# Kernel tuning notes

Hardware: AMD Instinct MI355X
Metric: run time of the kernel (lower is better)

## Reference

```python
import jax, jax.numpy as jnp
from jax import lax
import numpy as np

B, T, F = 64, 128, 16
H = 512
S = 2  # num_seg; SEG_DICT['2'] = [8, 6], seg_cumsum = [2, 10, 16]


def timestep_embedding(t, dim, max_period=10000.0):
    half = dim // 2
    freqs = jnp.exp(-jnp.log(max_period) * jnp.arange(half, dtype=jnp.float32) / half)
    args = t[:, None] * freqs  # [N, half]
    return jnp.concatenate([jnp.cos(args), jnp.sin(args)], axis=-1)  # [N, dim]


def setup_inputs() -> dict:
    key = jax.random.key(0)
    ks = jax.random.split(key, 16)
    sc = lambda *sh: 1.0 / np.sqrt(sh[-1])
    inp = {
        'x': jax.random.normal(ks[0], (B, T, F), dtype=jnp.float32),
        'lengths': jax.random.randint(ks[1], (B,), 1, T + 1),
        'h0': jax.random.uniform(ks[2], (B, H), dtype=jnp.float32),
        'c0': jax.random.uniform(ks[3], (B, H), dtype=jnp.float32),
        'W_is0': jax.random.normal(ks[4], (H, 8), dtype=jnp.float32) * sc(8),
        'b_is0': jax.random.normal(ks[5], (H,), dtype=jnp.float32) * 0.01,
        'W_is1': jax.random.normal(ks[6], (H, 6), dtype=jnp.float32) * sc(6),
        'b_is1': jax.random.normal(ks[7], (H,), dtype=jnp.float32) * 0.01,
        'W_ih': jax.random.normal(ks[8], (4 * H, 3 * H), dtype=jnp.float32) * sc(3 * H),
        'W_hh': jax.random.normal(ks[9], (4 * H, H), dtype=jnp.float32) * sc(H),
        'b_ih': jax.random.normal(ks[10], (4 * H,), dtype=jnp.float32) * 0.01,
        'b_hh': jax.random.normal(ks[11], (4 * H,), dtype=jnp.float32) * 0.01,
        'W_o': jax.random.normal(ks[12], (F - 2, S * H), dtype=jnp.float32) * sc(S * H),
        'b_o': jax.random.normal(ks[13], (F - 2,), dtype=jnp.float32) * 0.01,
    }
    return inp


def reference(x, lengths, h0, c0, W_is0, b_is0, W_is1, b_is1,
              W_ih, W_hh, b_ih, b_hh, W_o, b_o):
    b, t, f = x.shape
    h = h0.shape[1]
    xf = x.reshape(-1, f)  # [B*T, F]

    # timestep embeddings from the two time columns (learning_type='diff')
    tc = timestep_embedding(xf[:, 0], h)
    tp = timestep_embedding(xf[:, 1], h)
    t_emb = jnp.concatenate([tc, tp], axis=-1)  # [B*T, 2H]

    # per-segment input linears (segments = cols 2:10 and 10:16)
    e0 = xf[:, 2:10] @ W_is0.T + b_is0
    e1 = xf[:, 10:16] @ W_is1.T + b_is1
    e0 = jnp.concatenate([e0, t_emb], axis=-1)[:, None, :]  # [B*T, 1, 3H]
    e1 = jnp.concatenate([e1, t_emb], axis=-1)[:, None, :]
    # faithful to torch: concat on dim=1 then reshape(batch, num_seg, seq_len, -1)
    embs = jnp.concatenate([e0, e1], axis=1).reshape(b, S, t, 3 * h)

    def cell(carry, xt):
        hh, cc = carry
        gates = xt @ W_ih.T + b_ih + hh @ W_hh.T + b_hh
        i, fg, g, o = jnp.split(gates, 4, axis=-1)  # torch LSTMCell order i,f,g,o
        cc = jax.nn.sigmoid(fg) * cc + jax.nn.sigmoid(i) * jnp.tanh(g)
        hh = jax.nn.sigmoid(o) * jnp.tanh(cc)
        return (hh, cc), hh

    hs = []
    for s in range(S):  # shared cell weights across segments (same nn.LSTMCell object)
        xs = jnp.swapaxes(embs[:, s], 0, 1)  # [T, B, 3H]
        _, h_seq = lax.scan(cell, (h0, c0), xs)  # [T, B, H]
        hs.append(jnp.swapaxes(h_seq, 0, 1))  # [B, T, H]
    hidden_states = jnp.stack(hs, axis=-2)  # [B, T, S, H]; dropout rate 0 -> identity

    idx = lengths - 1  # final valid timestep per sequence
    hfin = hidden_states[jnp.arange(b), idx].reshape(b, S * h)  # [B, S*H]
    out = jax.nn.sigmoid(hfin @ W_o.T + b_o)  # mlp_o: Linear + Sigmoid
    return out
```

## Files before the change

kernel.cpp:

```cpp
#include <hip/hip_runtime.h>
#include <hip/hip_bf16.h>
#include <stdint.h>


typedef __attribute__((ext_vector_type(8))) short bf16x8_t;
typedef __attribute__((ext_vector_type(4))) float f32x4_t;

#define SENT 0xAAAAAAAAu

#define OFF_G      0u
#define OFF_TEMB   33554432u
#define OFF_HH     50331648u
#define OFF_WHH    67239936u
#define OFF_WMID   69337088u
#define OFF_WC0    73531392u
#define OFF_WC1    73596928u
#define OFF_BC     73662464u
#define OFF_HFIN   73678848u

__device__ __forceinline__ float bf2f(uint16_t u){
  union { uint32_t i; float f; } v; v.i = ((uint32_t)u) << 16; return v.f;
}
__device__ __forceinline__ uint16_t f2b(float f){
  union { float f; uint32_t i; } v; v.f = f;
  uint32_t r = v.i + 0x7fffu + ((v.i >> 16) & 1u);
  return (uint16_t)(r >> 16);
}
__device__ __forceinline__ float sigm(float x){ return 1.0f/(1.0f + __expf(-x)); }
__device__ __forceinline__ float tanh_(float x){
  float xc = fminf(fmaxf(x, -15.f), 15.f);
  float t = __expf(2.f*xc);
  return (t - 1.f)/(t + 1.f);
}
__device__ __forceinline__ void gl_lds16(const void* g, void* l){
  __builtin_amdgcn_global_load_lds(
      (const __attribute__((address_space(1))) void*)g,
      (__attribute__((address_space(3))) void*)l, 16, 0, 0);
}

__global__ void prep1(const float* __restrict__ W_ih, const float* __restrict__ W_hh,
                      const float* __restrict__ W_is0, const float* __restrict__ b_is0,
                      const float* __restrict__ W_is1, const float* __restrict__ b_is1,
                      const float* __restrict__ b_ih, const float* __restrict__ b_hh,
                      uint16_t* __restrict__ whh_b, uint16_t* __restrict__ wmid_b,
                      float* __restrict__ wc0, float* __restrict__ wc1, float* __restrict__ bc){
  const int n = blockIdx.x;
  const int tid = threadIdx.x;
  __shared__ float wrow[512];
  __shared__ float red[16][17];
  wrow[tid]       = W_ih[(size_t)n*1536 + tid];
  wrow[tid + 256] = W_ih[(size_t)n*1536 + 256 + tid];
  for (int j = tid; j < 1024; j += 256)
    wmid_b[(size_t)n*1024 + j] = f2b(W_ih[(size_t)n*1536 + 512 + j]);
  for (int k = tid; k < 512; k += 256)
    whh_b[(size_t)n*512 + k] = f2b(W_hh[(size_t)n*512 + k]);
  __syncthreads();
  {
    const int d = tid >> 4, jp = tid & 15;
    float s = 0.f;
    const int kk0 = jp*32;
    if (d < 8){
      for (int k = kk0; k < kk0 + 32; ++k) s += wrow[k]*W_is0[k*8 + d];
    } else if (d < 14){
      int c = d - 8;
      for (int k = kk0; k < kk0 + 32; ++k) s += wrow[k]*W_is1[k*6 + c];
    } else if (d == 14){
      for (int k = kk0; k < kk0 + 32; ++k) s += wrow[k]*b_is0[k];
    } else {
      for (int k = kk0; k < kk0 + 32; ++k) s += wrow[k]*b_is1[k];
    }
    red[d][jp] = s;
  }
  __syncthreads();
  if (tid < 16){
    float tot = 0.f;
    #pragma unroll
    for (int i = 0; i < 16; ++i) tot += red[tid][i];
    if (tid < 8)       wc0[n*8 + tid] = tot;
    else if (tid < 14) wc1[n*8 + (tid - 8)] = tot;
    else if (tid == 14) bc[n]        = b_ih[n] + b_hh[n] + tot;
    else                bc[2048 + n] = b_ih[n] + b_hh[n] + tot;
  } else if (tid == 16){
    wc1[n*8 + 6] = 0.f; wc1[n*8 + 7] = 0.f;
  }
}

__global__ void prep2(const float* __restrict__ h0, uint16_t* __restrict__ h_hist){
  int i = blockIdx.x*256 + threadIdx.x;
  uint32_t* hh = (uint32_t*)h_hist;
  if (i < 32768){
    int e    = i*2;
    int rrcg = e >> 9;
    int rr   = rrcg >> 4, cg = rrcg & 15;
    int rm   = e & 511;
    int row  = rm >> 5, u = rm & 31;
    int b    = (rr*16 + row) & 63;
    int unit = cg*32 + u;
    uint32_t lo = f2b(h0[(size_t)b*512 + unit]);
    uint32_t hi = f2b(h0[(size_t)b*512 + unit + 1]);
    uint32_t wd = lo | (hi << 16);
    if (wd == SENT) wd ^= 1u;
    hh[i] = wd;
  } else if (i < 4227072){
    hh[i] = SENT;
  }
}

__global__ void tembk(const float* __restrict__ x, uint16_t* __restrict__ temb){
  const int rid = blockIdx.x;
  const int k = threadIdx.x;
  float x0 = x[(size_t)rid*16 + 0], x1 = x[(size_t)rid*16 + 1];
  float f = __expf((float)k * (-9.210340371976184f/256.f));
  float a0 = x0*f, a1 = x1*f;
  size_t base = (size_t)rid*1024;
  temb[base + k]        = f2b(__cosf(a0));
  temb[base + 256 + k]  = f2b(__sinf(a0));
  temb[base + 512 + k]  = f2b(__cosf(a1));
  temb[base + 768 + k]  = f2b(__sinf(a1));
}

__launch_bounds__(256)
__global__ void gemmB(const uint16_t* __restrict__ temb, const uint16_t* __restrict__ wmid,
                      uint16_t* __restrict__ G){
  __shared__ __align__(16) uint16_t smem[16384];
  uint16_t* Al = smem;
  uint16_t* Bl = smem + 8192;
  const int tid = threadIdx.x;
  const int m0 = blockIdx.x*128, n0 = blockIdx.y*128;
  const int w = tid >> 6, lane = tid & 63;
  const int q = lane >> 4, ln = lane & 15;
  const int wm = w >> 1, wn = w & 1;
  const int srow_l = (lane >> 3);
  const int scol   = (lane & 7)*8;

  f32x4_t acc[4][4];
  #pragma unroll
  for (int a = 0; a < 4; ++a)
    #pragma unroll
    for (int b = 0; b < 4; ++b) acc[a][b] = (f32x4_t){0.f,0.f,0.f,0.f};

  for (int kb = 0; kb < 16; ++kb){
    #pragma unroll
    for (int i = 0; i < 4; ++i){
      int row0 = w*32 + i*8;
      int row  = row0 + srow_l;
      gl_lds16(temb + (size_t)(m0 + row)*1024 + kb*64 + scol, &Al[row0*64]);
      gl_lds16(wmid + (size_t)(n0 + row)*1024 + kb*64 + scol, &Bl[row0*64]);
    }
    __syncthreads();
    #pragma unroll
    for (int kc = 0; kc < 2; ++kc){
      bf16x8_t af[4], bf[4];
      #pragma unroll
      for (int mt = 0; mt < 4; ++mt)
        af[mt] = *(const bf16x8_t*)&Al[(wm*64 + mt*16 + ln)*64 + kc*32 + q*8];
      #pragma unroll
      for (int nt = 0; nt < 4; ++nt)
        bf[nt] = *(const bf16x8_t*)&Bl[(wn*64 + nt*16 + ln)*64 + kc*32 + q*8];
      #pragma unroll
      for (int mt = 0; mt < 4; ++mt)
        #pragma unroll
        for (int nt = 0; nt < 4; ++nt)
          acc[mt][nt] = __builtin_amdgcn_mfma_f32_16x16x32_bf16(af[mt], bf[nt], acc[mt][nt], 0, 0, 0);
    }
    __syncthreads();
  }

  #pragma unroll
  for (int mt = 0; mt < 4; ++mt)
    #pragma unroll
    for (int nt = 0; nt < 4; ++nt)
      #pragma unroll
      for (int r = 0; r < 4; ++r){
        int Mr = wm*64 + mt*16 + q*4 + r;
        int Nc = wn*64 + nt*16 + ln;
        smem[Mr*128 + Nc] = f2b(acc[mt][nt][r]);
      }
  __syncthreads();
  {
    const int erow = tid >> 1, eh = tid & 1;
    uint4* gdst = (uint4*)(G + (size_t)(m0 + erow)*2048 + n0 + eh*64);
    const uint4* lsrc = (const uint4*)&smem[erow*128 + eh*64];
    #pragma unroll
    for (int i2 = 0; i2 < 8; ++i2) gdst[i2] = lsrc[i2];
  }
}

__launch_bounds__(256)
__global__ void lstmk(const float* __restrict__ x, const float* __restrict__ c0,
                      const int* __restrict__ lengths,
                      const uint16_t* __restrict__ whh_b, const uint16_t* __restrict__ G,
                      const float* __restrict__ wc0, const float* __restrict__ wc1,
                      const float* __restrict__ bc,
                      uint16_t* __restrict__ h_hist, float* __restrict__ hfin){
  __shared__ __align__(16) uint16_t h_l[2][16][552];

  const int tid = threadIdx.x;
  const int bid = blockIdx.x;
  const int rr = bid & 7;
  const int g  = bid >> 3;
  const int k0 = g*32;
  const int sp = rr >> 2;
  const int w = tid >> 6, lane = tid & 63;
  const int q = lane >> 4, ln = lane & 15;
  const int u8 = ln & 7, gh = ln >> 3;
  const int unit = k0 + w*8 + u8;
  const int gl0 = gh*512 + unit;
  const int gl1 = (2 + gh)*512 + unit;

  const int LVL = 65536;

  bf16x8_t barr0[16], barr1[16];
  #pragma unroll
  for (int kc = 0; kc < 16; ++kc){
    barr0[kc] = *(const bf16x8_t*)(whh_b + (size_t)gl0*512 + kc*32 + q*8);
    barr1[kc] = *(const bf16x8_t*)(whh_b + (size_t)gl1*512 + kc*32 + q*8);
  }
  bf16x8_t e0f[2], e1f[2];
  #pragma unroll
  for (int nsI = 0; nsI < 2; ++nsI){
    bf16x8_t v0 = {0,0,0,0,0,0,0,0}, v1 = {0,0,0,0,0,0,0,0};
    if (q == 0){
      const float* wcs = nsI ? wc1 : wc0;
      #pragma unroll
      for (int jj = 0; jj < 8; ++jj){
        ((uint16_t*)&v0)[jj] = f2b(wcs[gl0*8 + jj]);
        ((uint16_t*)&v1)[jj] = f2b(wcs[gl1*8 + jj]);
      }
    }
    e0f[nsI] = v0; e1f[nsI] = v1;
  }
  float bc0v[2] = { bc[gl0], bc[2048 + gl0] };
  float bc1v[2] = { bc[gl1], bc[2048 + gl1] };

  int   bmr[4], lenr[4];
  float cst[4];
  #pragma unroll
  for (int r = 0; r < 4; ++r){
    int row = rr*16 + q*4 + r;
    bmr[r]  = row & 63;
    lenr[r] = lengths[bmr[r]];
    cst[r]  = c0[(size_t)bmr[r]*512 + unit];
  }

  const int prow = lane >> 2;
  const int pcol = (lane & 3)*8;
  const int xm = tid >> 3, xc = tid & 7;
  const int xb = (rr*16 + xm) & 63;

  const size_t stb = ((size_t)rr*8192 + g*512);

  for (int idx = tid; idx < 2*16*32; idx += 256)
    h_l[idx >> 9][(idx >> 5) & 15][520 + (idx & 31)] = 0;

  for (int t = 0; t < 128; ++t){
    const int qidx = sp*128 + t;
    const int ntm = qidx >> 1;
    const int ns  = qidx & 1;
    const int buf = t & 1;

    uint16_t g0r[4], g1r[4];
    #pragma unroll
    for (int r = 0; r < 4; ++r){
      size_t grow = (size_t)(bmr[r]*128 + ntm)*2048;
      g0r[r] = G[grow + gl0];
      g1r[r] = G[grow + gl1];
    }
    float xv = 0.f;
    if (tid < 128){
      if (ns == 0)      xv = x[(size_t)(xb*128 + ntm)*16 + 2 + xc];
      else if (xc < 6)  xv = x[(size_t)(xb*128 + ntm)*16 + 10 + xc];
    }

    {
      const unsigned long long* lvl = (const unsigned long long*)h_hist
                                      + (((size_t)t*LVL + (size_t)rr*8192) >> 2);
      unsigned long long hv[4][2];
      while (true){
        bool ok = true;
        #pragma unroll
        for (int i = 0; i < 4; ++i){
          const unsigned long long* p = lvl + ((size_t)(w*4 + i)*128 + prow*8 + (pcol >> 2));
          hv[i][0] = __hip_atomic_load(&p[0], __ATOMIC_RELAXED, __HIP_MEMORY_SCOPE_AGENT);
          hv[i][1] = __hip_atomic_load(&p[1], __ATOMIC_RELAXED, __HIP_MEMORY_SCOPE_AGENT);
          ok &= ((uint32_t)hv[i][0] != SENT) & ((uint32_t)(hv[i][0] >> 32) != SENT)
              & ((uint32_t)hv[i][1] != SENT) & ((uint32_t)(hv[i][1] >> 32) != SENT);
        }
        if (__all(ok)) break;
        __builtin_amdgcn_s_sleep(1);
      }
      #pragma unroll
      for (int i = 0; i < 4; ++i){
        int reg = w*4 + i;
        *(unsigned long long*)&h_l[buf][prow][reg*32 + pcol]     = hv[i][0];
        *(unsigned long long*)&h_l[buf][prow][reg*32 + pcol + 4] = hv[i][1];
      }
    }
    if (tid < 128) h_l[buf][xm][512 + xc] = f2b(xv);
    __syncthreads();

    f32x4_t acc0, acc1;
    {
      float b0 = ns ? bc0v[1] : bc0v[0];
      float b1 = ns ? bc1v[1] : bc1v[0];
      #pragma unroll
      for (int r = 0; r < 4; ++r){ acc0[r] = bf2f(g0r[r]) + b0; acc1[r] = bf2f(g1r[r]) + b1; }
    }
    #pragma unroll
    for (int kc = 0; kc < 16; ++kc){
      bf16x8_t a = *(const bf16x8_t*)&h_l[buf][ln][kc*32 + q*8];
      acc0 = __builtin_amdgcn_mfma_f32_16x16x32_bf16(a, barr0[kc], acc0, 0, 0, 0);
      acc1 = __builtin_amdgcn_mfma_f32_16x16x32_bf16(a, barr1[kc], acc1, 0, 0, 0);
    }
    {
      bf16x8_t a = *(const bf16x8_t*)&h_l[buf][ln][512 + q*8];
      acc0 = __builtin_amdgcn_mfma_f32_16x16x32_bf16(a, ns ? e0f[1] : e0f[0], acc0, 0, 0, 0);
      acc1 = __builtin_amdgcn_mfma_f32_16x16x32_bf16(a, ns ? e1f[1] : e1f[0], acc1, 0, 0, 0);
    }

    float pf[4], po[4];
    #pragma unroll
    for (int r = 0; r < 4; ++r){
      pf[r] = __shfl_xor(acc0[r], 8);
      po[r] = __shfl_xor(acc1[r], 8);
    }
    if (ln < 8){
      uint32_t hb[4]; float hF[4];
      #pragma unroll
      for (int r = 0; r < 4; ++r){
        float ig = acc0[r], fg = pf[r], gg = acc1[r], og = po[r];
        cst[r] = sigm(fg)*cst[r] + sigm(ig)*tanh_(gg);
        float h = sigm(og)*tanh_(cst[r]);
        hF[r] = h; hb[r] = (uint32_t)f2b(h);
      }
      #pragma unroll
      for (int r = 0; r < 4; ++r){
        uint32_t ph = (uint32_t)__shfl_xor((int)hb[r], 1);
        uint32_t packed = hb[r] | (ph << 16);
        if (packed == SENT) packed ^= 1u;
        uint32_t hi = (uint32_t)__shfl_xor((int)packed, 2);
        if ((ln & 3) == 0){
          unsigned long long v = (unsigned long long)packed | ((unsigned long long)hi << 32);
          unsigned long long* hp = (unsigned long long*)h_hist
              + (((size_t)(t+1)*LVL + stb + (size_t)(q*4 + r)*32 + w*8 + u8) >> 2);
          __hip_atomic_store(hp, v, __ATOMIC_RELAXED, __HIP_MEMORY_SCOPE_AGENT);
        }
        if (t == lenr[r] - 1)
          hfin[(size_t)bmr[r]*1024 + sp*512 + unit] = hF[r];
      }
    }
  }
}

__global__ void outk(const float* __restrict__ hfin, const float* __restrict__ W_o,
                     const float* __restrict__ b_o, float* __restrict__ out){
  __shared__ float hl[1024];
  __shared__ float red[16][17];
  const int b = blockIdx.x, tid = threadIdx.x;
  #pragma unroll
  for (int i = 0; i < 4; ++i) hl[tid + i*256] = hfin[(size_t)b*1024 + tid + i*256];
  __syncthreads();
  const int o = tid >> 4, j0 = tid & 15;
  float s = 0.f;
  if (o < 14){
    for (int j = j0; j < 1024; j += 16) s += hl[j]*W_o[(size_t)o*1024 + j];
  }
  red[o][j0] = s;
  __syncthreads();
  if (tid < 14){
    float tot = b_o[tid];
    #pragma unroll
    for (int i = 0; i < 16; ++i) tot += red[tid][i];
    out[b*14 + tid] = 1.0f/(1.0f + __expf(-tot));
  }
}

extern "C" void kernel_launch(void* const* d_in, const int* in_sizes, int n_in,
                              void* d_out, int out_size, void* d_ws, size_t ws_size,
                              hipStream_t stream){
  const float* x     = (const float*)d_in[0];
  const int*   lens  = (const int*)  d_in[1];
  const float* h0    = (const float*)d_in[2];
  const float* c0    = (const float*)d_in[3];
  const float* W_is0 = (const float*)d_in[4];
  const float* b_is0 = (const float*)d_in[5];
  const float* W_is1 = (const float*)d_in[6];
  const float* b_is1 = (const float*)d_in[7];
  const float* W_ih  = (const float*)d_in[8];
  const float* W_hh  = (const float*)d_in[9];
  const float* b_ih  = (const float*)d_in[10];
  const float* b_hh  = (const float*)d_in[11];
  const float* W_o   = (const float*)d_in[12];
  const float* b_o   = (const float*)d_in[13];
  float* out = (float*)d_out;

  char* ws = (char*)d_ws;
  uint16_t* G      = (uint16_t*)(ws + OFF_G);
  uint16_t* temb   = (uint16_t*)(ws + OFF_TEMB);
  uint16_t* h_hist = (uint16_t*)(ws + OFF_HH);
  uint16_t* whh_b  = (uint16_t*)(ws + OFF_WHH);
  uint16_t* wmid_b = (uint16_t*)(ws + OFF_WMID);
  float* wc0  = (float*)(ws + OFF_WC0);
  float* wc1  = (float*)(ws + OFF_WC1);
  float* bc   = (float*)(ws + OFF_BC);
  float* hfin = (float*)(ws + OFF_HFIN);

  hipLaunchKernelGGL(prep1, dim3(2048), dim3(256), 0, stream,
                     W_ih, W_hh, W_is0, b_is0, W_is1, b_is1, b_ih, b_hh,
                     whh_b, wmid_b, wc0, wc1, bc);
  hipLaunchKernelGGL(prep2, dim3(16512), dim3(256), 0, stream, h0, h_hist);
  hipLaunchKernelGGL(tembk, dim3(8192), dim3(256), 0, stream, x, temb);
  hipLaunchKernelGGL(gemmB, dim3(64, 16), dim3(256), 0, stream, temb, wmid_b, G);
  hipLaunchKernelGGL(lstmk, dim3(128), dim3(256), 0, stream,
                     x, c0, lens, whh_b, G, wc0, wc1, bc, h_hist, hfin);
  hipLaunchKernelGGL(outk, dim3(64), dim3(256), 0, stream, hfin, W_o, b_o, out);
}
```

Measured before the change: 590.4 us.

## Fuse GEMM into LSTM kernel with per-tile flags to overlap input projection

Merges the three prep kernels into one launch and folds the input-projection GEMM into the recurrent LSTM kernel. The first 128 blocks run the recurrence while the remaining blocks compute G tiles, each publishing a release flag that the recurrent blocks poll before consuming that tile. Tiles are reordered so timesteps needed first are produced early, and the G layout changes so rows are indexed by time then batch. This hides the GEMM behind the serial LSTM and removes launch gaps. The cost is spin-wait polling and a dependence on the GEMM blocks being scheduled alongside the persistent blocks.

After: 569.1 us. 1.04x faster.

```diff
diff --git a/kernel.cpp b/kernel.cpp
--- a/kernel.cpp
+++ b/kernel.cpp
@@ -17,6 +17,7 @@
 #define OFF_WC1    73596928u
 #define OFF_BC     73662464u
 #define OFF_HFIN   73678848u
+#define OFF_GFLAG  73940992u
 
 __device__ __forceinline__ float bf2f(uint16_t u){
   union { uint32_t i; float f; } v; v.i = ((uint32_t)u) << 16; return v.f;
@@ -38,57 +39,71 @@
       (__attribute__((address_space(3))) void*)l, 16, 0, 0);
 }
 
-__global__ void prep1(const float* __restrict__ W_ih, const float* __restrict__ W_hh,
-                      const float* __restrict__ W_is0, const float* __restrict__ b_is0,
-                      const float* __restrict__ W_is1, const float* __restrict__ b_is1,
-                      const float* __restrict__ b_ih, const float* __restrict__ b_hh,
-                      uint16_t* __restrict__ whh_b, uint16_t* __restrict__ wmid_b,
-                      float* __restrict__ wc0, float* __restrict__ wc1, float* __restrict__ bc){
-  const int n = blockIdx.x;
-  const int tid = threadIdx.x;
-  __shared__ float wrow[512];
-  __shared__ float red[16][17];
-  wrow[tid]       = W_ih[(size_t)n*1536 + tid];
-  wrow[tid + 256] = W_ih[(size_t)n*1536 + 256 + tid];
-  for (int j = tid; j < 1024; j += 256)
-    wmid_b[(size_t)n*1024 + j] = f2b(W_ih[(size_t)n*1536 + 512 + j]);
-  for (int k = tid; k < 512; k += 256)
-    whh_b[(size_t)n*512 + k] = f2b(W_hh[(size_t)n*512 + k]);
-  __syncthreads();
-  {
-    const int d = tid >> 4, jp = tid & 15;
-    float s = 0.f;
-    const int kk0 = jp*32;
-    if (d < 8){
-      for (int k = kk0; k < kk0 + 32; ++k) s += wrow[k]*W_is0[k*8 + d];
-    } else if (d < 14){
-      int c = d - 8;
-      for (int k = kk0; k < kk0 + 32; ++k) s += wrow[k]*W_is1[k*6 + c];
-    } else if (d == 14){
-      for (int k = kk0; k < kk0 + 32; ++k) s += wrow[k]*b_is0[k];
-    } else {
-      for (int k = kk0; k < kk0 + 32; ++k) s += wrow[k]*b_is1[k];
-    }
-    red[d][jp] = s;
-  }
-  __syncthreads();
-  if (tid < 16){
-    float tot = 0.f;
-    #pragma unroll
-    for (int i = 0; i < 16; ++i) tot += red[tid][i];
-    if (tid < 8)       wc0[n*8 + tid] = tot;
-    else if (tid < 14) wc1[n*8 + (tid - 8)] = tot;
-    else if (tid == 14) bc[n]        = b_ih[n] + b_hh[n] + tot;
-    else                bc[2048 + n] = b_ih[n] + b_hh[n] + tot;
-  } else if (tid == 16){
-    wc1[n*8 + 6] = 0.f; wc1[n*8 + 7] = 0.f;
-  }
-}
-
-__global__ void prep2(const float* __restrict__ h0, uint16_t* __restrict__ h_hist){
-  int i = blockIdx.x*256 + threadIdx.x;
-  uint32_t* hh = (uint32_t*)h_hist;
-  if (i < 32768){
+__global__ void prepAll(const float* __restrict__ x,
+                        const float* __restrict__ W_ih, const float* __restrict__ W_hh,
+                        const float* __restrict__ W_is0, const float* __restrict__ b_is0,
+                        const float* __restrict__ W_is1, const float* __restrict__ b_is1,
+                        const float* __restrict__ b_ih, const float* __restrict__ b_hh,
+                        const float* __restrict__ h0,
+                        uint16_t* __restrict__ whh_b, uint16_t* __restrict__ wmid_b,
+                        float* __restrict__ wc0, float* __restrict__ wc1,
+                        float* __restrict__ bc,
+                        uint16_t* __restrict__ temb, uint16_t* __restrict__ h_hist,
+                        uint32_t* __restrict__ gflag){
+  const int bid = blockIdx.x, tid = threadIdx.x;
+  if (bid < 2048){
+    const int n = bid;
+    __shared__ float wrow[512];
+    __shared__ float red[16][17];
+    wrow[tid]       = W_ih[(size_t)n*1536 + tid];
+    wrow[tid + 256] = W_ih[(size_t)n*1536 + 256 + tid];
+    for (int j = tid; j < 1024; j += 256)
+      wmid_b[(size_t)n*1024 + j] = f2b(W_ih[(size_t)n*1536 + 512 + j]);
+    for (int k = tid; k < 512; k += 256)
+      whh_b[(size_t)n*512 + k] = f2b(W_hh[(size_t)n*512 + k]);
+    __syncthreads();
+    {
+      const int d = tid >> 4, jp = tid & 15;
+      float s = 0.f;
+      const int kk0 = jp*32;
+      if (d < 8){
+        for (int k = kk0; k < kk0 + 32; ++k) s += wrow[k]*W_is0[k*8 + d];
+      } else if (d < 14){
+        int c = d - 8;
+        for (int k = kk0; k < kk0 + 32; ++k) s += wrow[k]*W_is1[k*6 + c];
+      } else if (d == 14){
+        for (int k = kk0; k < kk0 + 32; ++k) s += wrow[k]*b_is0[k];
+      } else {
+        for (int k = kk0; k < kk0 + 32; ++k) s += wrow[k]*b_is1[k];
+      }
+      red[d][jp] = s;
+    }
+    __syncthreads();
+    if (tid < 16){
+      float tot = 0.f;
+      #pragma unroll
+      for (int i = 0; i < 16; ++i) tot += red[tid][i];
+      if (tid < 8)        wc0[n*8 + tid] = tot;
+      else if (tid < 14)  wc1[n*8 + (tid - 8)] = tot;
+      else if (tid == 14) bc[n]        = b_ih[n] + b_hh[n] + tot;
+      else                bc[2048 + n] = b_ih[n] + b_hh[n] + tot;
+    } else if (tid == 16){
+      wc1[n*8 + 6] = 0.f; wc1[n*8 + 7] = 0.f;
+    }
+  } else if (bid < 10240){
+    const int rid = bid - 2048;
+    const int k = tid;
+    float x0 = x[(size_t)rid*16 + 0], x1 = x[(size_t)rid*16 + 1];
+    float f = __expf((float)k * (-9.210340371976184f/256.f));
+    float a0 = x0*f, a1 = x1*f;
+    size_t base = (size_t)rid*1024;
+    temb[base + k]        = f2b(__cosf(a0));
+    temb[base + 256 + k]  = f2b(__sinf(a0));
+    temb[base + 512 + k]  = f2b(__cosf(a1));
+    temb[base + 768 + k]  = f2b(__sinf(a1));
+  } else if (bid < 10368){
+    int i = (bid - 10240)*256 + tid;
+    uint32_t* hh = (uint32_t*)h_hist;
     int e    = i*2;
     int rrcg = e >> 9;
     int rr   = rrcg >> 4, cg = rrcg & 15;
@@ -101,113 +116,110 @@
     uint32_t wd = lo | (hi << 16);
     if (wd == SENT) wd ^= 1u;
     hh[i] = wd;
-  } else if (i < 4227072){
-    hh[i] = SENT;
-  }
-}
-
-__global__ void tembk(const float* __restrict__ x, uint16_t* __restrict__ temb){
-  const int rid = blockIdx.x;
-  const int k = threadIdx.x;
-  float x0 = x[(size_t)rid*16 + 0], x1 = x[(size_t)rid*16 + 1];
-  float f = __expf((float)k * (-9.210340371976184f/256.f));
-  float a0 = x0*f, a1 = x1*f;
-  size_t base = (size_t)rid*1024;
-  temb[base + k]        = f2b(__cosf(a0));
-  temb[base + 256 + k]  = f2b(__sinf(a0));
-  temb[base + 512 + k]  = f2b(__cosf(a1));
-  temb[base + 768 + k]  = f2b(__sinf(a1));
+    if (i < 1024) gflag[i] = 0u;
+  } else {
+    uint32_t* hh = (uint32_t*)h_hist;
+    size_t w0 = 32768u + ((size_t)(bid - 10368)*256 + tid)*8;
+    uint4 s4 = make_uint4(SENT, SENT, SENT, SENT);
+    *(uint4*)&hh[w0]     = s4;
+    *(uint4*)&hh[w0 + 4] = s4;
+  }
 }
 
 __launch_bounds__(256)
-__global__ void gemmB(const uint16_t* __restrict__ temb, const uint16_t* __restrict__ wmid,
-                      uint16_t* __restrict__ G){
-  __shared__ __align__(16) uint16_t smem[16384];
-  uint16_t* Al = smem;
-  uint16_t* Bl = smem + 8192;
+__global__ void fusedk(const float* __restrict__ x, const float* __restrict__ c0,
+                       const int* __restrict__ lengths,
+                       const uint16_t* __restrict__ whh_b, const uint16_t* __restrict__ temb,
+                       const uint16_t* __restrict__ wmid,
+                       const float* __restrict__ wc0, const float* __restrict__ wc1,
+                       const float* __restrict__ bc,
+                       uint16_t* __restrict__ G, uint16_t* __restrict__ h_hist,
+                       uint32_t* __restrict__ gflag, float* __restrict__ hfin){
+  __shared__ __align__(16) uint16_t smem_u[17664];
   const int tid = threadIdx.x;
-  const int m0 = blockIdx.x*128, n0 = blockIdx.y*128;
+  const int bid = blockIdx.x;
   const int w = tid >> 6, lane = tid & 63;
   const int q = lane >> 4, ln = lane & 15;
-  const int wm = w >> 1, wn = w & 1;
-  const int srow_l = (lane >> 3);
-  const int scol   = (lane & 7)*8;
-
-  f32x4_t acc[4][4];
-  #pragma unroll
-  for (int a = 0; a < 4; ++a)
-    #pragma unroll
-    for (int b = 0; b < 4; ++b) acc[a][b] = (f32x4_t){0.f,0.f,0.f,0.f};
-
-  for (int kb = 0; kb < 16; ++kb){
-    #pragma unroll
-    for (int i = 0; i < 4; ++i){
-      int row0 = w*32 + i*8;
-      int row  = row0 + srow_l;
-      gl_lds16(temb + (size_t)(m0 + row)*1024 + kb*64 + scol, &Al[row0*64]);
-      gl_lds16(wmid + (size_t)(n0 + row)*1024 + kb*64 + scol, &Bl[row0*64]);
-    }
+
+  if (bid >= 128){
+    const int gb = bid - 128;
+    const int idx = gb >> 4;
+    const int mt = (idx & 1) ? (idx >> 1) : (32 + (idx >> 1));
+    const int n0 = (gb & 15)*128;
+    uint16_t* Al = smem_u;
+    uint16_t* Bl = smem_u + 8192;
+    const int wm = w >> 1, wn = w & 1;
+    const int srow_l = lane >> 3, scol = (lane & 7)*8;
+
+    f32x4_t acc[4][4];
+    #pragma unroll
+    for (int a = 0; a < 4; ++a)
+      #pragma unroll
+      for (int b2 = 0; b2 < 4; ++b2) acc[a][b2] = (f32x4_t){0.f,0.f,0.f,0.f};
+
+    for (int kb = 0; kb < 16; ++kb){
+      #pragma unroll
+      for (int i = 0; i < 4; ++i){
+        int row0 = w*32 + i*8;
+        int lrow = row0 + srow_l;
+        int bA = lrow & 63, ntmA = mt*2 + (lrow >> 6);
+        gl_lds16(temb + (size_t)(bA*128 + ntmA)*1024 + kb*64 + scol, &Al[row0*64]);
+        gl_lds16(wmid + (size_t)(n0 + lrow)*1024 + kb*64 + scol, &Bl[row0*64]);
+      }
+      __syncthreads();
+      #pragma unroll
+      for (int kc = 0; kc < 2; ++kc){
+        bf16x8_t af[4], bf[4];
+        #pragma unroll
+        for (int mt_i = 0; mt_i < 4; ++mt_i)
+          af[mt_i] = *(const bf16x8_t*)&Al[(wm*64 + mt_i*16 + ln)*64 + kc*32 + q*8];
+        #pragma unroll
+        for (int nt = 0; nt < 4; ++nt)
+          bf[nt] = *(const bf16x8_t*)&Bl[(wn*64 + nt*16 + ln)*64 + kc*32 + q*8];
+        #pragma unroll
+        for (int mt_i = 0; mt_i < 4; ++mt_i)
+          #pragma unroll
+          for (int nt = 0; nt < 4; ++nt)
+            acc[mt_i][nt] = __builtin_amdgcn_mfma_f32_16x16x32_bf16(af[mt_i], bf[nt], acc[mt_i][nt], 0, 0, 0);
+      }
+      __syncthreads();
+    }
+    #pragma unroll
+    for (int mt_i = 0; mt_i < 4; ++mt_i)
+      #pragma unroll
+      for (int nt = 0; nt < 4; ++nt)
+        #pragma unroll
+        for (int r = 0; r < 4; ++r){
+          int Mr = wm*64 + mt_i*16 + q*4 + r;
+          int Nc = wn*64 + nt*16 + ln;
+          smem_u[Mr*128 + Nc] = f2b(acc[mt_i][nt][r]);
+        }
     __syncthreads();
-    #pragma unroll
-    for (int kc = 0; kc < 2; ++kc){
-      bf16x8_t af[4], bf[4];
-      #pragma unroll
-      for (int mt = 0; mt < 4; ++mt)
-        af[mt] = *(const bf16x8_t*)&Al[(wm*64 + mt*16 + ln)*64 + kc*32 + q*8];
-      #pragma unroll
-      for (int nt = 0; nt < 4; ++nt)
-        bf[nt] = *(const bf16x8_t*)&Bl[(wn*64 + nt*16 + ln)*64 + kc*32 + q*8];
-      #pragma unroll
-      for (int mt = 0; mt < 4; ++mt)
-        #pragma unroll
-        for (int nt = 0; nt < 4; ++nt)
-          acc[mt][nt] = __builtin_amdgcn_mfma_f32_16x16x32_bf16(af[mt], bf[nt], acc[mt][nt], 0, 0, 0);
+    {
+      const int erow = tid >> 1, eh = tid & 1;
+      const unsigned long long* lsrc = (const unsigned long long*)&smem_u[erow*128 + eh*64];
+      unsigned long long* gdst = (unsigned long long*)
+          (G + (size_t)(mt*128 + erow)*2048 + n0 + eh*64);
+      #pragma unroll
+      for (int i2 = 0; i2 < 16; ++i2)
+        __hip_atomic_store(&gdst[i2], lsrc[i2], __ATOMIC_RELAXED, __HIP_MEMORY_SCOPE_AGENT);
     }
     __syncthreads();
-  }
-
-  #pragma unroll
-  for (int mt = 0; mt < 4; ++mt)
-    #pragma unroll
-    for (int nt = 0; nt < 4; ++nt)
-      #pragma unroll
-      for (int r = 0; r < 4; ++r){
-        int Mr = wm*64 + mt*16 + q*4 + r;
-        int Nc = wn*64 + nt*16 + ln;
-        smem[Mr*128 + Nc] = f2b(acc[mt][nt][r]);
-      }
-  __syncthreads();
-  {
-    const int erow = tid >> 1, eh = tid & 1;
-    uint4* gdst = (uint4*)(G + (size_t)(m0 + erow)*2048 + n0 + eh*64);
-    const uint4* lsrc = (const uint4*)&smem[erow*128 + eh*64];
-    #pragma unroll
-    for (int i2 = 0; i2 < 8; ++i2) gdst[i2] = lsrc[i2];
-  }
-}
-
-__launch_bounds__(256)
-__global__ void lstmk(const float* __restrict__ x, const float* __restrict__ c0,
-                      const int* __restrict__ lengths,
-                      const uint16_t* __restrict__ whh_b, const uint16_t* __restrict__ G,
-                      const float* __restrict__ wc0, const float* __restrict__ wc1,
-                      const float* __restrict__ bc,
-                      uint16_t* __restrict__ h_hist, float* __restrict__ hfin){
-  __shared__ __align__(16) uint16_t h_l[2][16][552];
-
-  const int tid = threadIdx.x;
-  const int bid = blockIdx.x;
+    if (tid == 0)
+      __hip_atomic_store(&gflag[mt*16 + (gb & 15)], 1u,
+                         __ATOMIC_RELEASE, __HIP_MEMORY_SCOPE_AGENT);
+    return;
+  }
+
+  #define HL(b,r,c) smem_u[(((b)*16 + (r))*552) + (c)]
   const int rr = bid & 7;
   const int g  = bid >> 3;
   const int k0 = g*32;
   const int sp = rr >> 2;
-  const int w = tid >> 6, lane = tid & 63;
-  const int q = lane >> 4, ln = lane & 15;
   const int u8 = ln & 7, gh = ln >> 3;
   const int unit = k0 + w*8 + u8;
   const int gl0 = gh*512 + unit;
   const int gl1 = (2 + gh)*512 + unit;
-
   const int LVL = 65536;
 
   bf16x8_t barr0[16], barr1[16];
@@ -247,11 +259,10 @@
   const int pcol = (lane & 3)*8;
   const int xm = tid >> 3, xc = tid & 7;
   const int xb = (rr*16 + xm) & 63;
-
   const size_t stb = ((size_t)rr*8192 + g*512);
 
-  for (int idx = tid; idx < 2*16*32; idx += 256)
-    h_l[idx >> 9][(idx >> 5) & 15][520 + (idx & 31)] = 0;
+  for (int idx2 = tid; idx2 < 2*16*32; idx2 += 256)
+    HL(idx2 >> 9, (idx2 >> 5) & 15, 520 + (idx2 & 31)) = 0;
 
   for (int t = 0; t < 128; ++t){
     const int qidx = sp*128 + t;
@@ -259,10 +270,25 @@
     const int ns  = qidx & 1;
     const int buf = t & 1;
 
+    if ((t & 3) == 0){
+      const int mt = qidx >> 2;
+      const uint32_t* gf = gflag + mt*16 + (g >> 2);
+      while (true){
+        bool ok = true;
+        #pragma unroll
+        for (int j = 0; j < 4; ++j){
+          uint32_t v = __hip_atomic_load(&gf[j*4], __ATOMIC_RELAXED, __HIP_MEMORY_SCOPE_AGENT);
+          ok &= (v != 0u);
+        }
+        if (ok) break;
+        __builtin_amdgcn_s_sleep(1);
+      }
+    }
+
     uint16_t g0r[4], g1r[4];
     #pragma unroll
     for (int r = 0; r < 4; ++r){
-      size_t grow = (size_t)(bmr[r]*128 + ntm)*2048;
+      size_t grow = (size_t)(ntm*64 + bmr[r])*2048;
       g0r[r] = G[grow + gl0];
       g1r[r] = G[grow + gl1];
     }
@@ -292,11 +318,11 @@
       #pragma unroll
       for (int i = 0; i < 4; ++i){
         int reg = w*4 + i;
-        *(unsigned long long*)&h_l[buf][prow][reg*32 + pcol]     = hv[i][0];
-        *(unsigned long long*)&h_l[buf][prow][reg*32 + pcol + 4] = hv[i][1];
-      }
-    }
-    if (tid < 128) h_l[buf][xm][512 + xc] = f2b(xv);
+        *(unsigned long long*)&HL(buf, prow, reg*32 + pcol)     = hv[i][0];
+        *(unsigned long long*)&HL(buf, prow, reg*32 + pcol + 4) = hv[i][1];
+      }
+    }
+    if (tid < 128) HL(buf, xm, 512 + xc) = f2b(xv);
     __syncthreads();
 
     f32x4_t acc0, acc1;
@@ -308,12 +334,12 @@
     }
     #pragma unroll
     for (int kc = 0; kc < 16; ++kc){
-      bf16x8_t a = *(const bf16x8_t*)&h_l[buf][ln][kc*32 + q*8];
+      bf16x8_t a = *(const bf16x8_t*)&HL(buf, ln, kc*32 + q*8);
       acc0 = __builtin_amdgcn_mfma_f32_16x16x32_bf16(a, barr0[kc], acc0, 0, 0, 0);
       acc1 = __builtin_amdgcn_mfma_f32_16x16x32_bf16(a, barr1[kc], acc1, 0, 0, 0);
     }
     {
-      bf16x8_t a = *(const bf16x8_t*)&h_l[buf][ln][512 + q*8];
+      bf16x8_t a = *(const bf16x8_t*)&HL(buf, ln, 512 + q*8);
       acc0 = __builtin_amdgcn_mfma_f32_16x16x32_bf16(a, ns ? e0f[1] : e0f[0], acc0, 0, 0, 0);
       acc1 = __builtin_amdgcn_mfma_f32_16x16x32_bf16(a, ns ? e1f[1] : e1f[0], acc1, 0, 0, 0);
     }
@@ -350,6 +376,7 @@
       }
     }
   }
+  #undef HL
 }
 
 __global__ void outk(const float* __restrict__ hfin, const float* __restrict__ W_o,
@@ -404,14 +431,13 @@
   float* wc1  = (float*)(ws + OFF_WC1);
   float* bc   = (float*)(ws + OFF_BC);
   float* hfin = (float*)(ws + OFF_HFIN);
-
-  hipLaunchKernelGGL(prep1, dim3(2048), dim3(256), 0, stream,
-                     W_ih, W_hh, W_is0, b_is0, W_is1, b_is1, b_ih, b_hh,
-                     whh_b, wmid_b, wc0, wc1, bc);
-  hipLaunchKernelGGL(prep2, dim3(16512), dim3(256), 0, stream, h0, h_hist);
-  hipLaunchKernelGGL(tembk, dim3(8192), dim3(256), 0, stream, x, temb);
-  hipLaunchKernelGGL(gemmB, dim3(64, 16), dim3(256), 0, stream, temb, wmid_b, G);
-  hipLaunchKernelGGL(lstmk, dim3(128), dim3(256), 0, stream,
-                     x, c0, lens, whh_b, G, wc0, wc1, bc, h_hist, hfin);
+  uint32_t* gflag = (uint32_t*)(ws + OFF_GFLAG);
+
+  hipLaunchKernelGGL(prepAll, dim3(12416), dim3(256), 0, stream,
+                     x, W_ih, W_hh, W_is0, b_is0, W_is1, b_is1, b_ih, b_hh, h0,
+                     whh_b, wmid_b, wc0, wc1, bc, temb, h_hist, gflag);
+  hipLaunchKernelGGL(fusedk, dim3(1152), dim3(256), 0, stream,
+                     x, c0, lens, whh_b, temb, wmid_b, wc0, wc1, bc,
+                     G, h_hist, gflag, hfin);
   hipLaunchKernelGGL(outk, dim3(64), dim3(256), 0, stream, hfin, W_o, b_o, out);
 }
```
